# Performance work log

Hardware: AMD Instinct MI355X
Metric: run time of the kernel (lower is better)

## Reference

```python
import jax, jax.numpy as jnp
import numpy as np

K = 3          # hardcoded by .expand(-1, -1, 3, -1) in the original module
EPS = 1e-8


def setup_inputs() -> dict:
    key = jax.random.key(0)
    k1, k2, k3 = jax.random.split(key, 3)
    B, N, M, C = 8, 16384, 1024, 256
    return {
        "xyz": jax.random.normal(k1, (B, N, 3), dtype=jnp.float32),
        "centroid_xyz": jax.random.normal(k2, (B, M, 3), dtype=jnp.float32),
        "centroid_f": jax.random.normal(k3, (B, C, M), dtype=jnp.float32),
    }


def reference(xyz, centroid_xyz, centroid_f):
    # centroid_f: [B, C, M] -> [B, M, C] (matches f[-1].permute(0, 2, 1))
    cf = jnp.transpose(centroid_f, (0, 2, 1))
    x2 = jnp.sum(xyz * xyz, axis=-1)                     # [B, N]
    c2 = jnp.sum(centroid_xyz * centroid_xyz, axis=-1)   # [B, M]
    d2 = x2[:, :, None] + c2[:, None, :] - 2.0 * jnp.einsum(
        "bnd,bmd->bnm", xyz, centroid_xyz)               # [B, N, M]
    dist = jnp.sqrt(jnp.maximum(d2, 0.0))
    # k smallest distances (sorted ascending, like torch.topk largest=False)
    neg_dk, idx = jax.lax.top_k(-dist, K)                # [B, N, K]
    dk = -neg_dk
    # inverse-distance weights, normalized over k neighbors
    w = 1.0 / jnp.maximum(dk, EPS)
    w = w / jnp.sum(w, axis=-1, keepdims=True)           # [B, N, K]
    # gather neighbor features: [B, N, K, C]
    nf = jax.vmap(lambda f_b, i_b: f_b[i_b])(cf, idx)
    # weighted sum over neighbors -> [B, N, C]
    return jnp.sum(w[..., None] * nf, axis=2)
```

## Files before the change

### kernel.cpp

```cpp
#include <hip/hip_runtime.h>
#include <math.h>

constexpr int B_ = 8;
constexpr int N_ = 16384;
constexpr int M_ = 1024;
constexpr int C_ = 256;
constexpr int NCHUNK = 8;
constexpr int CHUNK = M_ / NCHUNK;
constexpr int KEEP = 4;
constexpr int TOPK_BLOCK = 1024;

#define INSERT4(P, u)                                              \
  {                                                                \
    const float o0 = P##0, o1 = P##1, o2 = P##2;                   \
    P##0 = fminf(o0, (u));                                         \
    P##1 = __builtin_amdgcn_fmed3f(o0, P##1, (u));                 \
    P##2 = __builtin_amdgcn_fmed3f(o1, P##2, (u));                 \
    P##3 = __builtin_amdgcn_fmed3f(o2, P##3, (u));                 \
  }

__global__ __launch_bounds__(256) void prep_kernel(
    const float* __restrict__ cxyz,
    const float* __restrict__ cf,
    float* __restrict__ csoa,
    float4* __restrict__ cpack,
    float* __restrict__ fT)
{
  __shared__ float tile[32][33];
  const int tx = threadIdx.x;
  const int ty = threadIdx.y;
  if (blockIdx.x < 32) {
    const int i = blockIdx.x * 256 + (ty * 32 + tx);
    if (i < B_ * M_) {
      const int b = i >> 10;
      const int m = i & (M_ - 1);
      const int chunk = m >> 7;
      const int mi = m & (CHUNK - 1);
      const int pair = mi >> 1;
      const int sub = mi & 1;
      const float x = cxyz[3 * i + 0];
      const float y = cxyz[3 * i + 1];
      const float z = cxyz[3 * i + 2];
      const float w = x * x + y * y + z * z;
      float* pb = csoa + ((((size_t)b * NCHUNK + chunk) * (CHUNK / 2)) + pair) * 8 + sub;
      pb[0] = x; pb[2] = y; pb[4] = z; pb[6] = w;
      cpack[i] = make_float4(x, y, z, w);
    }
  } else {
    const int bid = blockIdx.x - 32;
    const int m0 = (bid & 31) * 32;
    const int c0 = ((bid >> 5) & 7) * 32;
    const int b = bid >> 8;
    const float* fb = cf + (size_t)b * C_ * M_;
    float* ftb = fT + (size_t)b * M_ * C_;
#pragma unroll
    for (int j = 0; j < 32; j += 8)
      tile[ty + j][tx] = fb[(size_t)(c0 + ty + j) * M_ + (m0 + tx)];
    __syncthreads();
#pragma unroll
    for (int j = 0; j < 32; j += 8)
      ftb[(size_t)(m0 + ty + j) * C_ + (c0 + tx)] = tile[tx][ty + j];
  }
}

__global__ __launch_bounds__(TOPK_BLOCK) void topk_chunk_kernel(
    const float* __restrict__ xyz,
    const float* __restrict__ csoa,
    unsigned* __restrict__ cand)
{
  const int b = blockIdx.z;
  const int chunk = blockIdx.y;
  const int n = blockIdx.x * TOPK_BLOCK + threadIdx.x;
  const size_t p = (size_t)b * N_ + n;

  const float* __restrict__ cb =
      csoa + (((size_t)b * NCHUNK + chunk) * (CHUNK / 2)) * 8;

  const float* xp = xyz + p * 3;
  const float x0 = xp[0], x1 = xp[1], x2 = xp[2];
  const float nx0 = -2.f * x0, nx1 = -2.f * x1, nx2 = -2.f * x2;
  const float x2p1 = fmaf(x0, x0, fmaf(x1, x1, fmaf(x2, x2, 1.0f)));

  float A0 = INFINITY, A1 = INFINITY, A2 = INFINITY, A3 = INFINITY;
  float B0 = INFINITY, B1 = INFINITY, B2 = INFINITY, B3 = INFINITY;

#pragma unroll 8
  for (int i = 0; i < CHUNK / 2; ++i) {
    const float* pb = cb + i * 8;
    float tx = fmaf(nx0, pb[0], x2p1), ty = fmaf(nx0, pb[1], x2p1);
    tx = fmaf(nx1, pb[2], tx); ty = fmaf(nx1, pb[3], ty);
    tx = fmaf(nx2, pb[4], tx); ty = fmaf(nx2, pb[5], ty);
    tx += pb[6]; ty += pb[7];
    const float kx = __uint_as_float((__float_as_uint(tx) & 0xFFFFFF80u) | (unsigned)(2 * i));
    const float ky = __uint_as_float((__float_as_uint(ty) & 0xFFFFFF80u) | (unsigned)(2 * i + 1));
    INSERT4(A, kx);
    INSERT4(B, ky);
  }
  INSERT4(A, B0);
  INSERT4(A, B1);
  INSERT4(A, B2);
  INSERT4(A, B3);

  const unsigned i0 = __float_as_uint(A0) & 127u;
  const unsigned i1 = __float_as_uint(A1) & 127u;
  const unsigned i2 = __float_as_uint(A2) & 127u;
  const unsigned i3 = __float_as_uint(A3) & 127u;
  cand[p * NCHUNK + chunk] = i0 | (i1 << 8) | (i2 << 16) | (i3 << 24);
}

__global__ __launch_bounds__(256) void merge_kernel(
    const float* __restrict__ xyz,
    const float4* __restrict__ cpack,
    const unsigned* __restrict__ cand,
    int*   __restrict__ out_idx,
    float* __restrict__ out_w)
{
  const size_t p = (size_t)blockIdx.x * 256 + threadIdx.x;
  const int b = (int)(p >> 14);

  const float* xp = xyz + p * 3;
  const double x0d = (double)xp[0], x1d = (double)xp[1], x2d = (double)xp[2];
  const float4* __restrict__ cb = cpack + (size_t)b * M_;

  const uint4* cw4 = (const uint4*)(cand + p * NCHUNK);
  const uint4 ca = cw4[0], cb2 = cw4[1];
  unsigned words[NCHUNK] = {ca.x, ca.y, ca.z, ca.w, cb2.x, cb2.y, cb2.z, cb2.w};

  double D0 = 1e300, D1 = 1e300, D2 = 1e300;
  int I0 = 0, I1 = 0, I2 = 0;
#pragma unroll
  for (int ch = 0; ch < NCHUNK; ++ch) {
    const unsigned w = words[ch];
#pragma unroll
    for (int j = 0; j < KEEP; ++j) {
      const int m = ch * CHUNK + (int)((w >> (8 * j)) & 255u);
      const float4 c = cb[m];
      const double cx = (double)c.x, cy = (double)c.y, cz = (double)c.z;
      const double dot = x0d * cx + x1d * cy + x2d * cz;
      const double c2d = cx * cx + cy * cy + cz * cz;
      const double kd = c2d - 2.0 * dot;
      if (kd < D2) {
        if (kd < D1) {
          D2 = D1; I2 = I1;
          if (kd < D0) { D1 = D0; I1 = I0; D0 = kd; I0 = m; }
          else         { D1 = kd; I1 = m; }
        } else {
          D2 = kd; I2 = m;
        }
      }
    }
  }

  const double xx = x0d * x0d + x1d * x1d + x2d * x2d;
  const float d0 = sqrtf(fmaxf((float)(xx + D0), 0.0f));
  const float d1 = sqrtf(fmaxf((float)(xx + D1), 0.0f));
  const float d2 = sqrtf(fmaxf((float)(xx + D2), 0.0f));
  float w0 = 1.0f / fmaxf(d0, 1e-8f);
  float w1 = 1.0f / fmaxf(d1, 1e-8f);
  float w2 = 1.0f / fmaxf(d2, 1e-8f);
  const float wsum = w0 + w1 + w2;
  w0 /= wsum; w1 /= wsum; w2 /= wsum;

  const size_t o = p * 3;
  out_idx[o + 0] = I0; out_idx[o + 1] = I1; out_idx[o + 2] = I2;
  out_w[o + 0] = w0;   out_w[o + 1] = w1;   out_w[o + 2] = w2;
}

__global__ __launch_bounds__(256) void gather_kernel(
    const float* __restrict__ fT,
    const int*   __restrict__ idx,
    const float* __restrict__ w,
    float* __restrict__ out)
{
  const int wid  = threadIdx.x >> 6;
  const int lane = threadIdx.x & 63;
  const size_t p = (size_t)blockIdx.x * 4 + wid;
  const int b = (int)(p >> 14);

  const size_t o = p * 3;
  const int i0 = idx[o + 0], i1 = idx[o + 1], i2 = idx[o + 2];
  const float w0 = w[o + 0], w1 = w[o + 1], w2 = w[o + 2];

  const float4* f4 = (const float4*)(fT + (size_t)b * M_ * C_);
  float4 a = f4[(size_t)i0 * (C_ / 4) + lane];
  float4 bb = f4[(size_t)i1 * (C_ / 4) + lane];
  float4 c = f4[(size_t)i2 * (C_ / 4) + lane];

  float4 r;
  r.x = w0 * a.x + w1 * bb.x + w2 * c.x;
  r.y = w0 * a.y + w1 * bb.y + w2 * c.y;
  r.z = w0 * a.z + w1 * bb.z + w2 * c.z;
  r.w = w0 * a.w + w1 * bb.w + w2 * c.w;

  ((float4*)out)[p * (C_ / 4) + lane] = r;
}

extern "C" void kernel_launch(void* const* d_in, const int* in_sizes, int n_in,
                              void* d_out, int out_size, void* d_ws, size_t ws_size,
                              hipStream_t stream) {
  const float* xyz  = (const float*)d_in[0];
  const float* cxyz = (const float*)d_in[1];
  const float* cf   = (const float*)d_in[2];
  float* out = (float*)d_out;

  char* ws = (char*)d_ws;
  const size_t npts = (size_t)B_ * N_;

  int*    idxbuf = (int*)ws;
  float*  wbuf   = (float*)(ws + npts * 3 * sizeof(int));
  size_t  off    = npts * 3 * 8;
  float4* cpack  = (float4*)(ws + off);
  off += (size_t)B_ * M_ * sizeof(float4);
  float*  csoa   = (float*)(ws + off);
  off += (size_t)B_ * M_ * 4 * sizeof(float);
  off = (off + 15) & ~(size_t)15;
  char*   region = ws + off;
  unsigned* cand = (unsigned*)region;
  size_t cand_bytes = (npts * (size_t)NCHUNK * 4 + 255) & ~(size_t)255;
  float* fT = (float*)(region + cand_bytes);

  prep_kernel<<<dim3(32 + 2048), dim3(32, 8), 0, stream>>>(
      cxyz, cf, csoa, cpack, fT);
  topk_chunk_kernel<<<dim3(N_ / TOPK_BLOCK, NCHUNK, B_), TOPK_BLOCK, 0, stream>>>(
      xyz, csoa, cand);
  merge_kernel<<<(unsigned)(npts / 256), 256, 0, stream>>>(
      xyz, cpack, cand, idxbuf, wbuf);
  gather_kernel<<<(unsigned)(npts / 4), 256, 0, stream>>>(fT, idxbuf, wbuf, out);
}
```

Baseline: 94.51 us.

## Fuse merge with gather and software-pipeline topk and merge across batch groups

Merges the merge and gather kernels into one block type that computes indices and weights into shared memory and then gathers features, removing the idx/weight global round trip. It then runs a staged sequence of launches in which topk blocks for batches k+1 are interleaved (2:1) with merge/gather blocks for batches k, so compute-bound topk work overlaps memory-bound gather work. The cost is more launches (five instead of three) and a 1024-thread block shape for the merge path, where only 256 threads do the merge step.

```diff
diff --git a/kernel.cpp b/kernel.cpp
--- a/kernel.cpp
+++ b/kernel.cpp
@@ -9,6 +9,9 @@
 constexpr int CHUNK = M_ / NCHUNK;
 constexpr int KEEP = 4;
 constexpr int TOPK_BLOCK = 1024;
+constexpr int TKB_PER_B = (N_ / TOPK_BLOCK) * NCHUNK;
+constexpr int MG_PTS = 256;
+constexpr int MGB_PER_B = N_ / MG_PTS;
 
 #define INSERT4(P, u)                                              \
   {                                                                \
@@ -63,136 +66,146 @@
   }
 }
 
-__global__ __launch_bounds__(TOPK_BLOCK) void topk_chunk_kernel(
+__global__ __launch_bounds__(1024, 8) void step_kernel(
     const float* __restrict__ xyz,
     const float* __restrict__ csoa,
-    unsigned* __restrict__ cand)
+    const float4* __restrict__ cpack,
+    const float* __restrict__ fT,
+    unsigned* __restrict__ cand,
+    float* __restrict__ out,
+    int tk_b0, int tk_nb, int mg_b0, int mg_nb)
 {
-  const int b = blockIdx.z;
-  const int chunk = blockIdx.y;
-  const int n = blockIdx.x * TOPK_BLOCK + threadIdx.x;
-  const size_t p = (size_t)b * N_ + n;
-
-  const float* __restrict__ cb =
-      csoa + (((size_t)b * NCHUNK + chunk) * (CHUNK / 2)) * 8;
-
-  const float* xp = xyz + p * 3;
-  const float x0 = xp[0], x1 = xp[1], x2 = xp[2];
-  const float nx0 = -2.f * x0, nx1 = -2.f * x1, nx2 = -2.f * x2;
-  const float x2p1 = fmaf(x0, x0, fmaf(x1, x1, fmaf(x2, x2, 1.0f)));
-
-  float A0 = INFINITY, A1 = INFINITY, A2 = INFINITY, A3 = INFINITY;
-  float B0 = INFINITY, B1 = INFINITY, B2 = INFINITY, B3 = INFINITY;
+  const int T = tk_nb * TKB_PER_B;
+  const int G = mg_nb * MGB_PER_B;
+  const int bid = blockIdx.x;
+  bool is_mg; int rid;
+  if (G == 0)      { is_mg = false; rid = bid; }
+  else if (T == 0) { is_mg = true;  rid = bid; }
+  else {
+    is_mg = ((bid % 3) == 2);
+    rid = is_mg ? (bid / 3) : (bid - (bid + 1) / 3);
+  }
+
+  if (!is_mg) {
+    const int b = tk_b0 + (rid >> 7);
+    const int r = rid & 127;
+    const int chunk = r >> 4;
+    const int n = (r & 15) * TOPK_BLOCK + threadIdx.x;
+    const size_t p = (size_t)b * N_ + n;
+
+    const float* __restrict__ cb =
+        csoa + (((size_t)b * NCHUNK + chunk) * (CHUNK / 2)) * 8;
+
+    const float* xp = xyz + p * 3;
+    const float x0 = xp[0], x1 = xp[1], x2 = xp[2];
+    const float nx0 = -2.f * x0, nx1 = -2.f * x1, nx2 = -2.f * x2;
+    const float x2p1 = fmaf(x0, x0, fmaf(x1, x1, fmaf(x2, x2, 1.0f)));
+
+    float A0 = INFINITY, A1 = INFINITY, A2 = INFINITY, A3 = INFINITY;
+    float B0 = INFINITY, B1 = INFINITY, B2 = INFINITY, B3 = INFINITY;
 
 #pragma unroll 8
-  for (int i = 0; i < CHUNK / 2; ++i) {
-    const float* pb = cb + i * 8;
-    float tx = fmaf(nx0, pb[0], x2p1), ty = fmaf(nx0, pb[1], x2p1);
-    tx = fmaf(nx1, pb[2], tx); ty = fmaf(nx1, pb[3], ty);
-    tx = fmaf(nx2, pb[4], tx); ty = fmaf(nx2, pb[5], ty);
-    tx += pb[6]; ty += pb[7];
-    const float kx = __uint_as_float((__float_as_uint(tx) & 0xFFFFFF80u) | (unsigned)(2 * i));
-    const float ky = __uint_as_float((__float_as_uint(ty) & 0xFFFFFF80u) | (unsigned)(2 * i + 1));
-    INSERT4(A, kx);
-    INSERT4(B, ky);
-  }
-  INSERT4(A, B0);
-  INSERT4(A, B1);
-  INSERT4(A, B2);
-  INSERT4(A, B3);
-
-  const unsigned i0 = __float_as_uint(A0) & 127u;
-  const unsigned i1 = __float_as_uint(A1) & 127u;
-  const unsigned i2 = __float_as_uint(A2) & 127u;
-  const unsigned i3 = __float_as_uint(A3) & 127u;
-  cand[p * NCHUNK + chunk] = i0 | (i1 << 8) | (i2 << 16) | (i3 << 24);
-}
-
-__global__ __launch_bounds__(256) void merge_kernel(
-    const float* __restrict__ xyz,
-    const float4* __restrict__ cpack,
-    const unsigned* __restrict__ cand,
-    int*   __restrict__ out_idx,
-    float* __restrict__ out_w)
-{
-  const size_t p = (size_t)blockIdx.x * 256 + threadIdx.x;
-  const int b = (int)(p >> 14);
-
-  const float* xp = xyz + p * 3;
-  const double x0d = (double)xp[0], x1d = (double)xp[1], x2d = (double)xp[2];
-  const float4* __restrict__ cb = cpack + (size_t)b * M_;
-
-  const uint4* cw4 = (const uint4*)(cand + p * NCHUNK);
-  const uint4 ca = cw4[0], cb2 = cw4[1];
-  unsigned words[NCHUNK] = {ca.x, ca.y, ca.z, ca.w, cb2.x, cb2.y, cb2.z, cb2.w};
-
-  double D0 = 1e300, D1 = 1e300, D2 = 1e300;
-  int I0 = 0, I1 = 0, I2 = 0;
-#pragma unroll
-  for (int ch = 0; ch < NCHUNK; ++ch) {
-    const unsigned w = words[ch];
-#pragma unroll
-    for (int j = 0; j < KEEP; ++j) {
-      const int m = ch * CHUNK + (int)((w >> (8 * j)) & 255u);
-      const float4 c = cb[m];
-      const double cx = (double)c.x, cy = (double)c.y, cz = (double)c.z;
-      const double dot = x0d * cx + x1d * cy + x2d * cz;
-      const double c2d = cx * cx + cy * cy + cz * cz;
-      const double kd = c2d - 2.0 * dot;
-      if (kd < D2) {
-        if (kd < D1) {
-          D2 = D1; I2 = I1;
-          if (kd < D0) { D1 = D0; I1 = I0; D0 = kd; I0 = m; }
-          else         { D1 = kd; I1 = m; }
-        } else {
-          D2 = kd; I2 = m;
+    for (int i = 0; i < CHUNK / 2; ++i) {
+      const float* pb = cb + i * 8;
+      float tx = fmaf(nx0, pb[0], x2p1), ty = fmaf(nx0, pb[1], x2p1);
+      tx = fmaf(nx1, pb[2], tx); ty = fmaf(nx1, pb[3], ty);
+      tx = fmaf(nx2, pb[4], tx); ty = fmaf(nx2, pb[5], ty);
+      tx += pb[6]; ty += pb[7];
+      const float kx = __uint_as_float((__float_as_uint(tx) & 0xFFFFFF80u) | (unsigned)(2 * i));
+      const float ky = __uint_as_float((__float_as_uint(ty) & 0xFFFFFF80u) | (unsigned)(2 * i + 1));
+      INSERT4(A, kx);
+      INSERT4(B, ky);
+    }
+    INSERT4(A, B0);
+    INSERT4(A, B1);
+    INSERT4(A, B2);
+    INSERT4(A, B3);
+
+    const unsigned i0 = __float_as_uint(A0) & 127u;
+    const unsigned i1 = __float_as_uint(A1) & 127u;
+    const unsigned i2 = __float_as_uint(A2) & 127u;
+    const unsigned i3 = __float_as_uint(A3) & 127u;
+    cand[p * NCHUNK + chunk] = i0 | (i1 << 8) | (i2 << 16) | (i3 << 24);
+  } else {
+    __shared__ int   sI[MG_PTS * 3];
+    __shared__ float sW[MG_PTS * 3];
+    const int b = mg_b0 + (rid >> 6);
+    const size_t pbase = (size_t)b * N_ + (size_t)(rid & 63) * MG_PTS;
+    const int tid = threadIdx.x;
+
+    if (tid < MG_PTS) {
+      const size_t p = pbase + tid;
+      const float* xp = xyz + p * 3;
+      const double x0d = (double)xp[0], x1d = (double)xp[1], x2d = (double)xp[2];
+      const float4* __restrict__ cb = cpack + (size_t)b * M_;
+
+      const uint4* cw4 = (const uint4*)(cand + p * NCHUNK);
+      const uint4 ca = cw4[0], cb2 = cw4[1];
+      unsigned words[NCHUNK] = {ca.x, ca.y, ca.z, ca.w, cb2.x, cb2.y, cb2.z, cb2.w};
+
+      double D0 = 1e300, D1 = 1e300, D2 = 1e300;
+      int I0 = 0, I1 = 0, I2 = 0;
+#pragma unroll
+      for (int ch = 0; ch < NCHUNK; ++ch) {
+        const unsigned w = words[ch];
+#pragma unroll
+        for (int j = 0; j < KEEP; ++j) {
+          const int m = ch * CHUNK + (int)((w >> (8 * j)) & 255u);
+          const float4 c = cb[m];
+          const double cx = (double)c.x, cy = (double)c.y, cz = (double)c.z;
+          const double dot = x0d * cx + x1d * cy + x2d * cz;
+          const double c2d = cx * cx + cy * cy + cz * cz;
+          const double kd = c2d - 2.0 * dot;
+          if (kd < D2) {
+            if (kd < D1) {
+              D2 = D1; I2 = I1;
+              if (kd < D0) { D1 = D0; I1 = I0; D0 = kd; I0 = m; }
+              else         { D1 = kd; I1 = m; }
+            } else {
+              D2 = kd; I2 = m;
+            }
+          }
         }
       }
-    }
-  }
-
-  const double xx = x0d * x0d + x1d * x1d + x2d * x2d;
-  const float d0 = sqrtf(fmaxf((float)(xx + D0), 0.0f));
-  const float d1 = sqrtf(fmaxf((float)(xx + D1), 0.0f));
-  const float d2 = sqrtf(fmaxf((float)(xx + D2), 0.0f));
-  float w0 = 1.0f / fmaxf(d0, 1e-8f);
-  float w1 = 1.0f / fmaxf(d1, 1e-8f);
-  float w2 = 1.0f / fmaxf(d2, 1e-8f);
-  const float wsum = w0 + w1 + w2;
-  w0 /= wsum; w1 /= wsum; w2 /= wsum;
-
-  const size_t o = p * 3;
-  out_idx[o + 0] = I0; out_idx[o + 1] = I1; out_idx[o + 2] = I2;
-  out_w[o + 0] = w0;   out_w[o + 1] = w1;   out_w[o + 2] = w2;
-}
-
-__global__ __launch_bounds__(256) void gather_kernel(
-    const float* __restrict__ fT,
-    const int*   __restrict__ idx,
-    const float* __restrict__ w,
-    float* __restrict__ out)
-{
-  const int wid  = threadIdx.x >> 6;
-  const int lane = threadIdx.x & 63;
-  const size_t p = (size_t)blockIdx.x * 4 + wid;
-  const int b = (int)(p >> 14);
-
-  const size_t o = p * 3;
-  const int i0 = idx[o + 0], i1 = idx[o + 1], i2 = idx[o + 2];
-  const float w0 = w[o + 0], w1 = w[o + 1], w2 = w[o + 2];
-
-  const float4* f4 = (const float4*)(fT + (size_t)b * M_ * C_);
-  float4 a = f4[(size_t)i0 * (C_ / 4) + lane];
-  float4 bb = f4[(size_t)i1 * (C_ / 4) + lane];
-  float4 c = f4[(size_t)i2 * (C_ / 4) + lane];
-
-  float4 r;
-  r.x = w0 * a.x + w1 * bb.x + w2 * c.x;
-  r.y = w0 * a.y + w1 * bb.y + w2 * c.y;
-  r.z = w0 * a.z + w1 * bb.z + w2 * c.z;
-  r.w = w0 * a.w + w1 * bb.w + w2 * c.w;
-
-  ((float4*)out)[p * (C_ / 4) + lane] = r;
+
+      const double xx = x0d * x0d + x1d * x1d + x2d * x2d;
+      const float d0 = sqrtf(fmaxf((float)(xx + D0), 0.0f));
+      const float d1 = sqrtf(fmaxf((float)(xx + D1), 0.0f));
+      const float d2 = sqrtf(fmaxf((float)(xx + D2), 0.0f));
+      float w0 = 1.0f / fmaxf(d0, 1e-8f);
+      float w1 = 1.0f / fmaxf(d1, 1e-8f);
+      float w2 = 1.0f / fmaxf(d2, 1e-8f);
+      const float wsum = w0 + w1 + w2;
+      w0 /= wsum; w1 /= wsum; w2 /= wsum;
+
+      sI[tid * 3 + 0] = I0; sI[tid * 3 + 1] = I1; sI[tid * 3 + 2] = I2;
+      sW[tid * 3 + 0] = w0; sW[tid * 3 + 1] = w1; sW[tid * 3 + 2] = w2;
+    }
+    __syncthreads();
+
+    const int wid = tid >> 6;
+    const int lane = tid & 63;
+    const float4* __restrict__ f4 = (const float4*)(fT + (size_t)b * M_ * C_);
+#pragma unroll 4
+    for (int j = 0; j < MG_PTS / 16; ++j) {
+      const int li = wid * 16 + j;
+      const size_t p = pbase + li;
+      const int i0 = sI[li * 3 + 0], i1 = sI[li * 3 + 1], i2 = sI[li * 3 + 2];
+      const float w0 = sW[li * 3 + 0], w1 = sW[li * 3 + 1], w2 = sW[li * 3 + 2];
+
+      float4 a  = f4[(size_t)i0 * (C_ / 4) + lane];
+      float4 bb = f4[(size_t)i1 * (C_ / 4) + lane];
+      float4 c  = f4[(size_t)i2 * (C_ / 4) + lane];
+
+      float4 rr;
+      rr.x = w0 * a.x + w1 * bb.x + w2 * c.x;
+      rr.y = w0 * a.y + w1 * bb.y + w2 * c.y;
+      rr.z = w0 * a.z + w1 * bb.z + w2 * c.z;
+      rr.w = w0 * a.w + w1 * bb.w + w2 * c.w;
+
+      ((float4*)out)[p * (C_ / 4) + lane] = rr;
+    }
+  }
 }
 
 extern "C" void kernel_launch(void* const* d_in, const int* in_sizes, int n_in,
@@ -204,26 +217,25 @@
   float* out = (float*)d_out;
 
   char* ws = (char*)d_ws;
-  const size_t npts = (size_t)B_ * N_;
-
-  int*    idxbuf = (int*)ws;
-  float*  wbuf   = (float*)(ws + npts * 3 * sizeof(int));
-  size_t  off    = npts * 3 * 8;
-  float4* cpack  = (float4*)(ws + off);
-  off += (size_t)B_ * M_ * sizeof(float4);
-  float*  csoa   = (float*)(ws + off);
+  float4* cpack = (float4*)ws;
+  size_t off = (size_t)B_ * M_ * sizeof(float4);
+  float* csoa = (float*)(ws + off);
   off += (size_t)B_ * M_ * 4 * sizeof(float);
-  off = (off + 15) & ~(size_t)15;
-  char*   region = ws + off;
-  unsigned* cand = (unsigned*)region;
-  size_t cand_bytes = (npts * (size_t)NCHUNK * 4 + 255) & ~(size_t)255;
-  float* fT = (float*)(region + cand_bytes);
+  off = (off + 255) & ~(size_t)255;
+  unsigned* cand = (unsigned*)(ws + off);
+  off += ((size_t)B_ * N_ * NCHUNK * 4 + 255) & ~(size_t)255;
+  float* fT = (float*)(ws + off);
 
   prep_kernel<<<dim3(32 + 2048), dim3(32, 8), 0, stream>>>(
       cxyz, cf, csoa, cpack, fT);
-  topk_chunk_kernel<<<dim3(N_ / TOPK_BLOCK, NCHUNK, B_), TOPK_BLOCK, 0, stream>>>(
-      xyz, csoa, cand);
-  merge_kernel<<<(unsigned)(npts / 256), 256, 0, stream>>>(
-      xyz, cpack, cand, idxbuf, wbuf);
-  gather_kernel<<<(unsigned)(npts / 4), 256, 0, stream>>>(fT, idxbuf, wbuf, out);
+  step_kernel<<<dim3(2 * TKB_PER_B), 1024, 0, stream>>>(
+      xyz, csoa, cpack, fT, cand, out, 0, 2, 0, 0);
+  step_kernel<<<dim3(2 * TKB_PER_B + 2 * MGB_PER_B), 1024, 0, stream>>>(
+      xyz, csoa, cpack, fT, cand, out, 2, 2, 0, 2);
+  step_kernel<<<dim3(2 * TKB_PER_B + 2 * MGB_PER_B), 1024, 0, stream>>>(
+      xyz, csoa, cpack, fT, cand, out, 4, 2, 2, 2);
+  step_kernel<<<dim3(2 * TKB_PER_B + 2 * MGB_PER_B), 1024, 0, stream>>>(
+      xyz, csoa, cpack, fT, cand, out, 6, 2, 4, 2);
+  step_kernel<<<dim3(2 * MGB_PER_B), 1024, 0, stream>>>(
+      xyz, csoa, cpack, fT, cand, out, 0, 0, 6, 2);
 }
```

Result: slower. 167.6 us (+77.3%).
